# Optimization experiments

Hardware: AMD Instinct MI355X
Metric: run time of the kernel (lower is better)

The kernel has to match this reference:

```python
import jax, jax.numpy as jnp
import numpy as np

N_NODES = 50000
HIDDEN = 64
N_EDGES = 1200000


def setup_inputs() -> dict:
    key = jax.random.key(0)
    ks = jax.random.split(key, 12)
    x = jax.random.normal(ks[0], (N_NODES, HIDDEN), dtype=jnp.float32)
    edge_index = jax.random.randint(ks[1], (2, N_EDGES), 0, N_NODES, dtype=jnp.int64)
    s = 1.0 / np.sqrt(HIDDEN)
    # RGCN layer (single relation): relation weight, root weight, bias
    W_rel1 = jax.random.normal(ks[2], (HIDDEN, HIDDEN), dtype=jnp.float32) * s
    W_root1 = jax.random.normal(ks[3], (HIDDEN, HIDDEN), dtype=jnp.float32) * s
    b1 = jnp.zeros((HIDDEN,), dtype=jnp.float32)
    # Three GraphConv layers: self weight, neighbor weight, bias each
    W_self2 = jax.random.normal(ks[4], (HIDDEN, HIDDEN), dtype=jnp.float32) * s
    W_nbr2 = jax.random.normal(ks[5], (HIDDEN, HIDDEN), dtype=jnp.float32) * s
    b2 = jnp.zeros((HIDDEN,), dtype=jnp.float32)
    W_self3 = jax.random.normal(ks[6], (HIDDEN, HIDDEN), dtype=jnp.float32) * s
    W_nbr3 = jax.random.normal(ks[7], (HIDDEN, HIDDEN), dtype=jnp.float32) * s
    b3 = jnp.zeros((HIDDEN,), dtype=jnp.float32)
    W_self4 = jax.random.normal(ks[8], (HIDDEN, HIDDEN), dtype=jnp.float32) * s
    W_nbr4 = jax.random.normal(ks[9], (HIDDEN, HIDDEN), dtype=jnp.float32) * s
    b4 = jnp.zeros((HIDDEN,), dtype=jnp.float32)
    return {
        "x": x, "edge_index": edge_index,
        "W_rel1": W_rel1, "W_root1": W_root1, "b1": b1,
        "W_self2": W_self2, "W_nbr2": W_nbr2, "b2": b2,
        "W_self3": W_self3, "W_nbr3": W_nbr3, "b3": b3,
        "W_self4": W_self4, "W_nbr4": W_nbr4, "b4": b4,
    }


def _rgcn(x, W_rel, W_root, b, src, dst, n_nodes):
    # single-relation RGCN: root transform + mean-aggregated relation transform
    msg = x[src] @ W_rel                                   # [E, H]
    agg = jax.ops.segment_sum(msg, dst, num_segments=n_nodes)
    cnt = jax.ops.segment_sum(jnp.ones((src.shape[0],), x.dtype), dst, num_segments=n_nodes)
    agg = agg / jnp.maximum(cnt, 1.0)[:, None]
    return x @ W_root + agg + b


def _graphconv(x, W_self, W_nbr, b, src, dst, n_nodes):
    # GraphConv: self transform + sum-aggregated neighbor transform
    agg = jax.ops.segment_sum(x[src], dst, num_segments=n_nodes)  # [N, H]
    return x @ W_self + agg @ W_nbr + b


def reference(x, edge_index, W_rel1, W_root1, b1, W_self2, W_nbr2, b2,
              W_self3, W_nbr3, b3, W_self4, W_nbr4, b4):
    n = x.shape[0]
    src, dst = edge_index[0], edge_index[1]
    h = jax.nn.relu(_rgcn(x, W_rel1, W_root1, b1, src, dst, n))
    h = jax.nn.relu(_graphconv(h, W_self2, W_nbr2, b2, src, dst, n))
    x_1 = h
    h = jax.nn.relu(_graphconv(h, W_self3, W_nbr3, b3, src, dst, n))
    h = jax.nn.relu(_graphconv(h, W_self4, W_nbr4, b4, src, dst, n))
    x_2 = h
    return (x_1, x_2)
```

## Files before the change

### kernel.cpp

```cpp
#include <hip/hip_runtime.h>

#define N_NODES 50000
#define HIDDEN  64
#define N_EDGES 1200000

#define BSHIFT 7
#define BUKSZ  128
#define NBUK   391
#define GBIN   256
#define PAD2   4096

__device__ __forceinline__ float bcastf(float v, int k) {
    return __int_as_float(__builtin_amdgcn_readlane(__float_as_int(v), k));
}

__device__ __forceinline__ unsigned short f2bf(float x) {
    unsigned u = __float_as_uint(x);
    u += 0x7fffu + ((u >> 16) & 1u);
    return (unsigned short)(u >> 16);
}

__device__ __forceinline__ float bfl(unsigned w) { return __uint_as_float(w << 16); }
__device__ __forceinline__ float bfh(unsigned w) { return __uint_as_float(w & 0xffff0000u); }


__global__ __launch_bounds__(512) void init_kernel(int* __restrict__ cursor) {
    int tid = threadIdx.x;
    if (tid < NBUK) cursor[tid] = tid * PAD2;
}

__global__ __launch_bounds__(256) void scatter_fused_kernel(const int* __restrict__ ei,
                                                            int* __restrict__ cursor,
                                                            int* __restrict__ tmp, int E) {
    __shared__ int h[NBUK];
    __shared__ int cur[NBUK];
    int tid = threadIdx.x;
    for (int b = tid; b < NBUK; b += 256) h[b] = 0;
    __syncthreads();
    for (int e = blockIdx.x * 256 + tid; e < E; e += GBIN * 256)
        atomicAdd(&h[ei[E + e] >> BSHIFT], 1);
    __syncthreads();
    for (int b = tid; b < NBUK; b += 256) cur[b] = atomicAdd(&cursor[b], h[b]);
    __syncthreads();
    for (int e = blockIdx.x * 256 + tid; e < E; e += GBIN * 256) {
        int src = ei[e];
        int dst = ei[E + e];
        int p = atomicAdd(&cur[dst >> BSHIFT], 1);
        tmp[p] = src | ((dst & (BUKSZ - 1)) << 16);
    }
}

__global__ __launch_bounds__(512) void bucketize_kernel(const int* __restrict__ tmp,
                                                        const int* __restrict__ cursor,
                                                        int2* __restrict__ row_info,
                                                        unsigned short* __restrict__ csr,
                                                        int n) {
    __shared__ int hist[BUKSZ];
    __shared__ int cur[BUKSZ];
    __shared__ unsigned short stage[PAD2];
    int b = blockIdx.x, tid = threadIdx.x;
    int base = b * PAD2;
    int count = cursor[b] - base;
    int node_base = b << BSHIFT;

    if (tid < BUKSZ) hist[tid] = 0;
    __syncthreads();
    for (int i = tid; i < count; i += 512)
        atomicAdd(&hist[tmp[base + i] >> 16], 1);
    __syncthreads();
    int v = (tid < BUKSZ) ? hist[tid] : 0;
#pragma unroll
    for (int o = 1; o < BUKSZ; o <<= 1) {
        __syncthreads();
        int y = (tid >= o && tid < BUKSZ) ? hist[tid - o] : 0;
        __syncthreads();
        if (tid < BUKSZ) hist[tid] += y;
    }
    __syncthreads();
    if (tid < BUKSZ) {
        int excl = hist[tid] - v;
        cur[tid] = excl;
        int node = node_base + tid;
        if (node < n) row_info[node] = make_int2(base + excl, v);
    }
    __syncthreads();
    for (int i = tid; i < count; i += 512) {
        int p = tmp[base + i];
        int slot = atomicAdd(&cur[p >> 16], 1);
        stage[slot] = (unsigned short)(p & 0xFFFF);
    }
    __syncthreads();
    for (int i = tid; i < count; i += 512)
        csr[base + i] = stage[i];
}

__global__ __launch_bounds__(256) void gemm2_kernel(const float* __restrict__ h,
                                                    const float* __restrict__ Wnbr,
                                                    const float* __restrict__ Wself,
                                                    const float* __restrict__ bias,
                                                    unsigned short* __restrict__ tbf,
                                                    float* __restrict__ u, int n) {
    int lane = threadIdx.x & 63;
    float wn[64], ws[64];
#pragma unroll
    for (int k = 0; k < 64; ++k) {
        wn[k] = Wnbr[k * 64 + lane];
        ws[k] = Wself[k * 64 + lane];
    }
    float bv = bias[lane];
    int wave = (blockIdx.x * 256 + threadIdx.x) >> 6;
    int nwaves = gridDim.x * 4;
    if (wave == 0) tbf[(size_t)n * 64 + lane] = 0;
    for (int i = wave; i < n; i += nwaves) {
        float hv = h[i * 64 + lane];
        float tacc = 0.f, uacc = bv;
#pragma unroll
        for (int k = 0; k < 64; ++k) {
            float hk = bcastf(hv, k);
            tacc = fmaf(hk, wn[k], tacc);
            uacc = fmaf(hk, ws[k], uacc);
        }
        tbf[(size_t)i * 64 + lane] = f2bf(tacc);
        u[(size_t)i * 64 + lane] = uacc;
    }
}

__global__ __launch_bounds__(256) void agg_kernel(const unsigned short* __restrict__ tbf,
                                                  const float* __restrict__ u,
                                                  const int2* __restrict__ row_info,
                                                  const unsigned short* __restrict__ csr,
                                                  float* __restrict__ out, int n, int use_mean) {
    int lane = threadIdx.x & 63;
    int g = lane >> 4;
    int q = lane & 15;
    int node = (blockIdx.x * 256 + threadIdx.x) >> 6;
    if (node >= n) return;
    int2 ri = row_info[node];
    int start = ri.x, deg = ri.y;
    float4 a0 = {0,0,0,0}, a1 = {0,0,0,0}, a2 = {0,0,0,0}, a3 = {0,0,0,0};
    float4 a4 = {0,0,0,0}, a5 = {0,0,0,0}, a6 = {0,0,0,0}, a7 = {0,0,0,0};
    for (int e = 0; e < deg; e += 64) {
        int cnt = deg - e;
        if (cnt > 64) cnt = 64;
        int idx = (lane < cnt) ? (int)csr[start + e + lane] : n;
        int cnt32 = (cnt + 31) & ~31;
        for (int j = 0; j < cnt32; j += 32) {
            int s0 = __shfl(idx, j + g);
            int s1 = __shfl(idx, j + 4 + g);
            int s2 = __shfl(idx, j + 8 + g);
            int s3 = __shfl(idx, j + 12 + g);
            int s4 = __shfl(idx, j + 16 + g);
            int s5 = __shfl(idx, j + 20 + g);
            int s6 = __shfl(idx, j + 24 + g);
            int s7 = __shfl(idx, j + 28 + g);
            const uint2 w0 = *(const uint2*)(tbf + (size_t)s0 * 64 + q * 4);
            const uint2 w1 = *(const uint2*)(tbf + (size_t)s1 * 64 + q * 4);
            const uint2 w2 = *(const uint2*)(tbf + (size_t)s2 * 64 + q * 4);
            const uint2 w3 = *(const uint2*)(tbf + (size_t)s3 * 64 + q * 4);
            const uint2 w4 = *(const uint2*)(tbf + (size_t)s4 * 64 + q * 4);
            const uint2 w5 = *(const uint2*)(tbf + (size_t)s5 * 64 + q * 4);
            const uint2 w6 = *(const uint2*)(tbf + (size_t)s6 * 64 + q * 4);
            const uint2 w7 = *(const uint2*)(tbf + (size_t)s7 * 64 + q * 4);
            a0.x += bfl(w0.x); a0.y += bfh(w0.x); a0.z += bfl(w0.y); a0.w += bfh(w0.y);
            a1.x += bfl(w1.x); a1.y += bfh(w1.x); a1.z += bfl(w1.y); a1.w += bfh(w1.y);
            a2.x += bfl(w2.x); a2.y += bfh(w2.x); a2.z += bfl(w2.y); a2.w += bfh(w2.y);
            a3.x += bfl(w3.x); a3.y += bfh(w3.x); a3.z += bfl(w3.y); a3.w += bfh(w3.y);
            a4.x += bfl(w4.x); a4.y += bfh(w4.x); a4.z += bfl(w4.y); a4.w += bfh(w4.y);
            a5.x += bfl(w5.x); a5.y += bfh(w5.x); a5.z += bfl(w5.y); a5.w += bfh(w5.y);
            a6.x += bfl(w6.x); a6.y += bfh(w6.x); a6.z += bfl(w6.y); a6.w += bfh(w6.y);
            a7.x += bfl(w7.x); a7.y += bfh(w7.x); a7.z += bfl(w7.y); a7.w += bfh(w7.y);
        }
    }
    float4 acc;
    acc.x = ((a0.x + a1.x) + (a2.x + a3.x)) + ((a4.x + a5.x) + (a6.x + a7.x));
    acc.y = ((a0.y + a1.y) + (a2.y + a3.y)) + ((a4.y + a5.y) + (a6.y + a7.y));
    acc.z = ((a0.z + a1.z) + (a2.z + a3.z)) + ((a4.z + a5.z) + (a6.z + a7.z));
    acc.w = ((a0.w + a1.w) + (a2.w + a3.w)) + ((a4.w + a5.w) + (a6.w + a7.w));
    acc.x += __shfl_xor(acc.x, 16); acc.y += __shfl_xor(acc.y, 16);
    acc.z += __shfl_xor(acc.z, 16); acc.w += __shfl_xor(acc.w, 16);
    acc.x += __shfl_xor(acc.x, 32); acc.y += __shfl_xor(acc.y, 32);
    acc.z += __shfl_xor(acc.z, 32); acc.w += __shfl_xor(acc.w, 32);

    float scale = 1.f;
    if (use_mean) scale = 1.f / fmaxf((float)deg, 1.f);
    if (g == 0) {
        const float4 uv = *(const float4*)(u + (size_t)node * 64 + q * 4);
        float4 r;
        r.x = fmaxf(uv.x + acc.x * scale, 0.f);
        r.y = fmaxf(uv.y + acc.y * scale, 0.f);
        r.z = fmaxf(uv.z + acc.z * scale, 0.f);
        r.w = fmaxf(uv.w + acc.w * scale, 0.f);
        *(float4*)(out + (size_t)node * 64 + q * 4) = r;
    }
}


extern "C" void kernel_launch(void* const* d_in, const int* in_sizes, int n_in,
                              void* d_out, int out_size, void* d_ws, size_t ws_size,
                              hipStream_t stream) {
    const float* x      = (const float*)d_in[0];
    const int*   ei     = (const int*)d_in[1];
    const float* Wrel1  = (const float*)d_in[2];
    const float* Wroot1 = (const float*)d_in[3];
    const float* b1     = (const float*)d_in[4];
    const float* Wself2 = (const float*)d_in[5];
    const float* Wnbr2  = (const float*)d_in[6];
    const float* b2     = (const float*)d_in[7];
    const float* Wself3 = (const float*)d_in[8];
    const float* Wnbr3  = (const float*)d_in[9];
    const float* b3     = (const float*)d_in[10];
    const float* Wself4 = (const float*)d_in[11];
    const float* Wnbr4  = (const float*)d_in[12];
    const float* b4     = (const float*)d_in[13];

    const int N = N_NODES, E = N_EDGES;

    auto align = [](size_t o) { return (o + 255) & ~(size_t)255; };
    char* base = (char*)d_ws;
    size_t off = 0;
    int*  cursor   = (int*)(base + off);  off = align(off + (size_t)NBUK * 4);
    int2* row_info = (int2*)(base + off); off = align(off + (size_t)N_NODES * 8);
    int*  tmp      = (int*)(base + off);  off = align(off + (size_t)NBUK * PAD2 * 4);
    unsigned short* csr = (unsigned short*)(base + off); off = align(off + (size_t)NBUK * PAD2 * 2);
    unsigned short* tbf = (unsigned short*)(base + off); off = align(off + (size_t)(N + 1) * 64 * 2);
    float* u  = (float*)(base + off); off = align(off + (size_t)N * 64 * 4);
    float* h1 = (float*)(base + off); off = align(off + (size_t)N * 64 * 4);

    float* out1 = (float*)d_out;
    float* out2 = (float*)d_out + (size_t)N * 64;

    init_kernel<<<1, 512, 0, stream>>>(cursor);
    scatter_fused_kernel<<<GBIN, 256, 0, stream>>>(ei, cursor, tmp, E);
    bucketize_kernel<<<NBUK, 512, 0, stream>>>(tmp, cursor, row_info, csr, N);

    const int GB = 768;
    const int AB = (N + 3) / 4;

    gemm2_kernel<<<GB, 256, 0, stream>>>(x, Wrel1, Wroot1, b1, tbf, u, N);
    agg_kernel<<<AB, 256, 0, stream>>>(tbf, u, row_info, csr, h1, N, 1);
    gemm2_kernel<<<GB, 256, 0, stream>>>(h1, Wnbr2, Wself2, b2, tbf, u, N);
    agg_kernel<<<AB, 256, 0, stream>>>(tbf, u, row_info, csr, out1, N, 0);
    gemm2_kernel<<<GB, 256, 0, stream>>>(out1, Wnbr3, Wself3, b3, tbf, u, N);
    agg_kernel<<<AB, 256, 0, stream>>>(tbf, u, row_info, csr, h1, N, 0);
    gemm2_kernel<<<GB, 256, 0, stream>>>(h1, Wnbr4, Wself4, b4, tbf, u, N);
    agg_kernel<<<AB, 256, 0, stream>>>(tbf, u, row_info, csr, out2, N, 0);
}
```

Baseline: 336.1 us.

## Fuse aggregation with next-layer GEMM and merge CSR build with first GEMM

Replaces the separate gemm and aggregation kernels with a fused kernel that aggregates neighbours, applies relu, then immediately computes the next layer's two projections from registers using bf16 weights held in LDS. The CSR build changes from a global-atomic cursor scatter to a two-pass chunked scheme with per-chunk, per-bucket start and count matrices. It also overlaps the first GEMM and weight packing with the graph-build blocks in the same launches. This cuts the launch count and avoids writing and re-reading intermediate activations through global memory. In exchange the weights are rounded to bf16, the serial per-thread loops in build_b may be unbalanced, and the fused kernel uses a fixed grid-stride layout.

Result: slower. 616.1 us (+83.3%).

```diff
diff --git a/kernel.cpp b/kernel.cpp
--- a/kernel.cpp
+++ b/kernel.cpp
@@ -7,142 +7,184 @@
 #define BSHIFT 7
 #define BUKSZ  128
 #define NBUK   391
-#define GBIN   256
+#define ABLK   512
+#define CH     2344
 #define PAD2   4096
+#define FBLK   1024
+#define NW     (FBLK * 4)
 
 __device__ __forceinline__ float bcastf(float v, int k) {
     return __int_as_float(__builtin_amdgcn_readlane(__float_as_int(v), k));
 }
-
-__device__ __forceinline__ unsigned short f2bf(float x) {
+__device__ __forceinline__ unsigned f2bf(float x) {
     unsigned u = __float_as_uint(x);
     u += 0x7fffu + ((u >> 16) & 1u);
-    return (unsigned short)(u >> 16);
-}
-
+    return u >> 16;
+}
 __device__ __forceinline__ float bfl(unsigned w) { return __uint_as_float(w << 16); }
 __device__ __forceinline__ float bfh(unsigned w) { return __uint_as_float(w & 0xffff0000u); }
-
-
-__global__ __launch_bounds__(512) void init_kernel(int* __restrict__ cursor) {
-    int tid = threadIdx.x;
-    if (tid < NBUK) cursor[tid] = tid * PAD2;
-}
-
-__global__ __launch_bounds__(256) void scatter_fused_kernel(const int* __restrict__ ei,
-                                                            int* __restrict__ cursor,
-                                                            int* __restrict__ tmp, int E) {
-    __shared__ int h[NBUK];
+__device__ __forceinline__ void bfly(float4& a) {
+    a.x += __shfl_xor(a.x, 16); a.y += __shfl_xor(a.y, 16);
+    a.z += __shfl_xor(a.z, 16); a.w += __shfl_xor(a.w, 16);
+    a.x += __shfl_xor(a.x, 32); a.y += __shfl_xor(a.y, 32);
+    a.z += __shfl_xor(a.z, 32); a.w += __shfl_xor(a.w, 32);
+}
+
+__global__ __launch_bounds__(512) void build_a_kernel(const int* __restrict__ ei,
+                                                      int* __restrict__ tmp,
+                                                      int* __restrict__ starts_m,
+                                                      int* __restrict__ counts_m,
+                                                      const float* __restrict__ Wn2, const float* __restrict__ Ws2,
+                                                      const float* __restrict__ Wn3, const float* __restrict__ Ws3,
+                                                      const float* __restrict__ Wn4, const float* __restrict__ Ws4,
+                                                      uint4* __restrict__ pw) {
+    __shared__ int hist[NBUK];
     __shared__ int cur[NBUK];
-    int tid = threadIdx.x;
-    for (int b = tid; b < NBUK; b += 256) h[b] = 0;
-    __syncthreads();
-    for (int e = blockIdx.x * 256 + tid; e < E; e += GBIN * 256)
-        atomicAdd(&h[ei[E + e] >> BSHIFT], 1);
-    __syncthreads();
-    for (int b = tid; b < NBUK; b += 256) cur[b] = atomicAdd(&cursor[b], h[b]);
-    __syncthreads();
-    for (int e = blockIdx.x * 256 + tid; e < E; e += GBIN * 256) {
-        int src = ei[e];
-        int dst = ei[E + e];
-        int p = atomicAdd(&cur[dst >> BSHIFT], 1);
-        tmp[p] = src | ((dst & (BUKSZ - 1)) << 16);
-    }
-}
-
-__global__ __launch_bounds__(512) void bucketize_kernel(const int* __restrict__ tmp,
-                                                        const int* __restrict__ cursor,
-                                                        int2* __restrict__ row_info,
-                                                        unsigned short* __restrict__ csr,
-                                                        int n) {
+    __shared__ int stage[CH];
+    int b = blockIdx.x, tid = threadIdx.x;
+    if (b < ABLK) {
+        int base = b * CH;
+        int cnt = N_EDGES - base; if (cnt > CH) cnt = CH;
+        for (int i = tid; i < NBUK; i += 512) hist[i] = 0;
+        __syncthreads();
+        for (int i = tid; i < cnt; i += 512)
+            atomicAdd(&hist[ei[N_EDGES + base + i] >> BSHIFT], 1);
+        __syncthreads();
+        int v = (tid < NBUK) ? hist[tid] : 0;
+#pragma unroll
+        for (int o = 1; o < NBUK; o <<= 1) {
+            __syncthreads();
+            int y = (tid >= o && tid < NBUK) ? hist[tid - o] : 0;
+            __syncthreads();
+            if (tid < NBUK) hist[tid] += y;
+        }
+        __syncthreads();
+        if (tid < NBUK) {
+            int excl = hist[tid] - v;
+            cur[tid] = excl;
+            starts_m[tid * ABLK + b] = base + excl;
+            counts_m[tid * ABLK + b] = v;
+        }
+        __syncthreads();
+        for (int i = tid; i < cnt; i += 512) {
+            int src = ei[base + i];
+            int dst = ei[N_EDGES + base + i];
+            int p = atomicAdd(&cur[dst >> BSHIFT], 1);
+            stage[p] = src | ((dst & (BUKSZ - 1)) << 16);
+        }
+        __syncthreads();
+        for (int i = tid; i < cnt; i += 512) tmp[base + i] = stage[i];
+    } else {
+        int layer = b - ABLK;
+        const float* Wn = (layer == 0) ? Wn2 : (layer == 1) ? Wn3 : Wn4;
+        const float* Ws = (layer == 0) ? Ws2 : (layer == 1) ? Ws3 : Ws4;
+        for (int e = tid; e < 1024; e += 512) {
+            const float4 a = *(const float4*)(Wn + e * 4);
+            const float4 c = *(const float4*)(Ws + e * 4);
+            uint4 o;
+            o.x = f2bf(a.x) | (f2bf(a.y) << 16);
+            o.y = f2bf(a.z) | (f2bf(a.w) << 16);
+            o.z = f2bf(c.x) | (f2bf(c.y) << 16);
+            o.w = f2bf(c.z) | (f2bf(c.w) << 16);
+            pw[layer * 1024 + e] = o;
+        }
+    }
+}
+
+__global__ __launch_bounds__(512) void build_b_kernel(const int* __restrict__ tmp,
+                                                      const int* __restrict__ starts_m,
+                                                      const int* __restrict__ counts_m,
+                                                      int2* __restrict__ row_info,
+                                                      unsigned short* __restrict__ csr,
+                                                      const float* __restrict__ x,
+                                                      const float* __restrict__ Wrel,
+                                                      const float* __restrict__ Wroot,
+                                                      const float* __restrict__ bias,
+                                                      unsigned short* __restrict__ tbf,
+                                                      float* __restrict__ u) {
+    __shared__ int sl[ABLK];
+    __shared__ int cl[ABLK];
     __shared__ int hist[BUKSZ];
     __shared__ int cur[BUKSZ];
     __shared__ unsigned short stage[PAD2];
     int b = blockIdx.x, tid = threadIdx.x;
-    int base = b * PAD2;
-    int count = cursor[b] - base;
-    int node_base = b << BSHIFT;
-
-    if (tid < BUKSZ) hist[tid] = 0;
-    __syncthreads();
-    for (int i = tid; i < count; i += 512)
-        atomicAdd(&hist[tmp[base + i] >> 16], 1);
-    __syncthreads();
-    int v = (tid < BUKSZ) ? hist[tid] : 0;
-#pragma unroll
-    for (int o = 1; o < BUKSZ; o <<= 1) {
-        __syncthreads();
-        int y = (tid >= o && tid < BUKSZ) ? hist[tid - o] : 0;
-        __syncthreads();
-        if (tid < BUKSZ) hist[tid] += y;
-    }
-    __syncthreads();
-    if (tid < BUKSZ) {
-        int excl = hist[tid] - v;
-        cur[tid] = excl;
-        int node = node_base + tid;
-        if (node < n) row_info[node] = make_int2(base + excl, v);
-    }
-    __syncthreads();
-    for (int i = tid; i < count; i += 512) {
-        int p = tmp[base + i];
-        int slot = atomicAdd(&cur[p >> 16], 1);
-        stage[slot] = (unsigned short)(p & 0xFFFF);
-    }
-    __syncthreads();
-    for (int i = tid; i < count; i += 512)
-        csr[base + i] = stage[i];
-}
-
-__global__ __launch_bounds__(256) void gemm2_kernel(const float* __restrict__ h,
-                                                    const float* __restrict__ Wnbr,
-                                                    const float* __restrict__ Wself,
-                                                    const float* __restrict__ bias,
-                                                    unsigned short* __restrict__ tbf,
-                                                    float* __restrict__ u, int n) {
-    int lane = threadIdx.x & 63;
-    float wn[64], ws[64];
-#pragma unroll
-    for (int k = 0; k < 64; ++k) {
-        wn[k] = Wnbr[k * 64 + lane];
-        ws[k] = Wself[k * 64 + lane];
-    }
-    float bv = bias[lane];
-    int wave = (blockIdx.x * 256 + threadIdx.x) >> 6;
-    int nwaves = gridDim.x * 4;
-    if (wave == 0) tbf[(size_t)n * 64 + lane] = 0;
-    for (int i = wave; i < n; i += nwaves) {
-        float hv = h[i * 64 + lane];
-        float tacc = 0.f, uacc = bv;
+    if (b < NBUK) {
+        sl[tid] = starts_m[b * ABLK + tid];
+        cl[tid] = counts_m[b * ABLK + tid];
+        if (tid < BUKSZ) hist[tid] = 0;
+        __syncthreads();
+        {
+            int s = sl[tid], c = cl[tid];
+            for (int i = 0; i < c; ++i) atomicAdd(&hist[tmp[s + i] >> 16], 1);
+        }
+        __syncthreads();
+        int v = (tid < BUKSZ) ? hist[tid] : 0;
+#pragma unroll
+        for (int o = 1; o < BUKSZ; o <<= 1) {
+            __syncthreads();
+            int y = (tid >= o && tid < BUKSZ) ? hist[tid - o] : 0;
+            __syncthreads();
+            if (tid < BUKSZ) hist[tid] += y;
+        }
+        __syncthreads();
+        if (tid < BUKSZ) {
+            int excl = hist[tid] - v;
+            cur[tid] = excl;
+            int node = (b << BSHIFT) + tid;
+            if (node < N_NODES) row_info[node] = make_int2(b * PAD2 + excl, v);
+        }
+        __syncthreads();
+        {
+            int s = sl[tid], c = cl[tid];
+            for (int i = 0; i < c; ++i) {
+                int p = tmp[s + i];
+                int slot = atomicAdd(&cur[p >> 16], 1);
+                stage[slot] = (unsigned short)(p & 0xFFFF);
+            }
+        }
+        __syncthreads();
+        int total = hist[BUKSZ - 1];
+        for (int i = tid; i < total; i += 512) csr[b * PAD2 + i] = stage[i];
+    } else {
+        int lane = tid & 63;
+        float wn[64], ws[64];
 #pragma unroll
         for (int k = 0; k < 64; ++k) {
-            float hk = bcastf(hv, k);
-            tacc = fmaf(hk, wn[k], tacc);
-            uacc = fmaf(hk, ws[k], uacc);
-        }
-        tbf[(size_t)i * 64 + lane] = f2bf(tacc);
-        u[(size_t)i * 64 + lane] = uacc;
-    }
-}
-
-__global__ __launch_bounds__(256) void agg_kernel(const unsigned short* __restrict__ tbf,
-                                                  const float* __restrict__ u,
-                                                  const int2* __restrict__ row_info,
-                                                  const unsigned short* __restrict__ csr,
-                                                  float* __restrict__ out, int n, int use_mean) {
-    int lane = threadIdx.x & 63;
-    int g = lane >> 4;
-    int q = lane & 15;
-    int node = (blockIdx.x * 256 + threadIdx.x) >> 6;
-    if (node >= n) return;
+            wn[k] = Wrel[k * 64 + lane];
+            ws[k] = Wroot[k * 64 + lane];
+        }
+        float bv = bias[lane];
+        int wave = (b - NBUK) * 8 + (tid >> 6);
+        int nwaves = (gridDim.x - NBUK) * 8;
+        if (wave == 0) tbf[(size_t)N_NODES * 64 + lane] = 0;
+        for (int i = wave; i < N_NODES; i += nwaves) {
+            float hv = x[i * 64 + lane];
+            float tacc = 0.f, uacc = bv;
+#pragma unroll
+            for (int k = 0; k < 64; ++k) {
+                float hk = bcastf(hv, k);
+                tacc = fmaf(hk, wn[k], tacc);
+                uacc = fmaf(hk, ws[k], uacc);
+            }
+            tbf[(size_t)i * 64 + lane] = (unsigned short)f2bf(tacc);
+            u[(size_t)i * 64 + lane] = uacc;
+        }
+    }
+}
+
+__device__ __forceinline__ float4 agg_node(const unsigned short* __restrict__ tin,
+                                           const float* __restrict__ uin,
+                                           const int2* __restrict__ row_info,
+                                           const unsigned short* __restrict__ csr,
+                                           int node, int lane, int g, int q, int use_mean) {
+    if (node >= N_NODES) return make_float4(0.f, 0.f, 0.f, 0.f);
     int2 ri = row_info[node];
     int start = ri.x, deg = ri.y;
-    float4 a0 = {0,0,0,0}, a1 = {0,0,0,0}, a2 = {0,0,0,0}, a3 = {0,0,0,0};
-    float4 a4 = {0,0,0,0}, a5 = {0,0,0,0}, a6 = {0,0,0,0}, a7 = {0,0,0,0};
+    float4 a0{0,0,0,0}, a1{0,0,0,0}, a2{0,0,0,0}, a3{0,0,0,0};
+    float4 a4{0,0,0,0}, a5{0,0,0,0}, a6{0,0,0,0}, a7{0,0,0,0};
     for (int e = 0; e < deg; e += 64) {
-        int cnt = deg - e;
-        if (cnt > 64) cnt = 64;
-        int idx = (lane < cnt) ? (int)csr[start + e + lane] : n;
+        int cnt = deg - e; if (cnt > 64) cnt = 64;
+        int idx = (lane < cnt) ? (int)csr[start + e + lane] : N_NODES;
         int cnt32 = (cnt + 31) & ~31;
         for (int j = 0; j < cnt32; j += 32) {
             int s0 = __shfl(idx, j + g);
@@ -153,14 +195,14 @@
             int s5 = __shfl(idx, j + 20 + g);
             int s6 = __shfl(idx, j + 24 + g);
             int s7 = __shfl(idx, j + 28 + g);
-            const uint2 w0 = *(const uint2*)(tbf + (size_t)s0 * 64 + q * 4);
-            const uint2 w1 = *(const uint2*)(tbf + (size_t)s1 * 64 + q * 4);
-            const uint2 w2 = *(const uint2*)(tbf + (size_t)s2 * 64 + q * 4);
-            const uint2 w3 = *(const uint2*)(tbf + (size_t)s3 * 64 + q * 4);
-            const uint2 w4 = *(const uint2*)(tbf + (size_t)s4 * 64 + q * 4);
-            const uint2 w5 = *(const uint2*)(tbf + (size_t)s5 * 64 + q * 4);
-            const uint2 w6 = *(const uint2*)(tbf + (size_t)s6 * 64 + q * 4);
-            const uint2 w7 = *(const uint2*)(tbf + (size_t)s7 * 64 + q * 4);
+            const uint2 w0 = *(const uint2*)(tin + (size_t)s0 * 64 + q * 4);
+            const uint2 w1 = *(const uint2*)(tin + (size_t)s1 * 64 + q * 4);
+            const uint2 w2 = *(const uint2*)(tin + (size_t)s2 * 64 + q * 4);
+            const uint2 w3 = *(const uint2*)(tin + (size_t)s3 * 64 + q * 4);
+            const uint2 w4 = *(const uint2*)(tin + (size_t)s4 * 64 + q * 4);
+            const uint2 w5 = *(const uint2*)(tin + (size_t)s5 * 64 + q * 4);
+            const uint2 w6 = *(const uint2*)(tin + (size_t)s6 * 64 + q * 4);
+            const uint2 w7 = *(const uint2*)(tin + (size_t)s7 * 64 + q * 4);
             a0.x += bfl(w0.x); a0.y += bfh(w0.x); a0.z += bfl(w0.y); a0.w += bfh(w0.y);
             a1.x += bfl(w1.x); a1.y += bfh(w1.x); a1.z += bfl(w1.y); a1.w += bfh(w1.y);
             a2.x += bfl(w2.x); a2.y += bfh(w2.x); a2.z += bfl(w2.y); a2.w += bfh(w2.y);
@@ -176,24 +218,93 @@
     acc.y = ((a0.y + a1.y) + (a2.y + a3.y)) + ((a4.y + a5.y) + (a6.y + a7.y));
     acc.z = ((a0.z + a1.z) + (a2.z + a3.z)) + ((a4.z + a5.z) + (a6.z + a7.z));
     acc.w = ((a0.w + a1.w) + (a2.w + a3.w)) + ((a4.w + a5.w) + (a6.w + a7.w));
-    acc.x += __shfl_xor(acc.x, 16); acc.y += __shfl_xor(acc.y, 16);
-    acc.z += __shfl_xor(acc.z, 16); acc.w += __shfl_xor(acc.w, 16);
-    acc.x += __shfl_xor(acc.x, 32); acc.y += __shfl_xor(acc.y, 32);
-    acc.z += __shfl_xor(acc.z, 32); acc.w += __shfl_xor(acc.w, 32);
-
-    float scale = 1.f;
-    if (use_mean) scale = 1.f / fmaxf((float)deg, 1.f);
-    if (g == 0) {
-        const float4 uv = *(const float4*)(u + (size_t)node * 64 + q * 4);
-        float4 r;
-        r.x = fmaxf(uv.x + acc.x * scale, 0.f);
-        r.y = fmaxf(uv.y + acc.y * scale, 0.f);
-        r.z = fmaxf(uv.z + acc.z * scale, 0.f);
-        r.w = fmaxf(uv.w + acc.w * scale, 0.f);
-        *(float4*)(out + (size_t)node * 64 + q * 4) = r;
-    }
-}
-
+    bfly(acc);
+    float sc = use_mean ? 1.f / fmaxf((float)deg, 1.f) : 1.f;
+    const float4 uv = *(const float4*)(uin + (size_t)node * 64 + q * 4);
+    float4 h;
+    h.x = fmaxf(uv.x + acc.x * sc, 0.f);
+    h.y = fmaxf(uv.y + acc.y * sc, 0.f);
+    h.z = fmaxf(uv.z + acc.z * sc, 0.f);
+    h.w = fmaxf(uv.w + acc.w * sc, 0.f);
+    return h;
+}
+
+__global__ __launch_bounds__(256) void fused_kernel(const unsigned short* __restrict__ tin,
+                                                    const float* __restrict__ uin,
+                                                    const int2* __restrict__ row_info,
+                                                    const unsigned short* __restrict__ csr,
+                                                    const uint4* __restrict__ pwL,
+                                                    const float* __restrict__ bias_next,
+                                                    unsigned short* __restrict__ tout,
+                                                    float* __restrict__ uout,
+                                                    float* __restrict__ dout,
+                                                    int use_mean, int do_gemm) {
+    __shared__ uint4 wlds[1024];
+    __shared__ float blds[64];
+    int tid = threadIdx.x;
+    if (do_gemm) {
+        for (int i = tid; i < 1024; i += 256) wlds[i] = pwL[i];
+        if (tid < 64) blds[tid] = bias_next[tid];
+        if (blockIdx.x == 0 && tid < 32)
+            ((uint4*)(tout + (size_t)N_NODES * 64))[tid % 8 + (tid / 8) * 0] = make_uint4(0,0,0,0);
+        if (blockIdx.x == 0 && tid < 64)
+            ((unsigned int*)(tout + (size_t)N_NODES * 64))[tid] = 0;
+    }
+    __syncthreads();
+    int lane = tid & 63, g = lane >> 4, q = lane & 15;
+    int w = blockIdx.x * 4 + (tid >> 6);
+
+#pragma unroll
+    for (int bi = 0; bi < 4; ++bi) {
+        int nodes[4];
+        float4 h4[4];
+#pragma unroll
+        for (int i = 0; i < 4; ++i) {
+            int node = w + NW * (bi * 4 + i);
+            nodes[i] = node;
+            h4[i] = agg_node(tin, uin, row_info, csr, node, lane, g, q, use_mean);
+            if (dout && node < N_NODES && g == 0)
+                *(float4*)(dout + (size_t)node * 64 + q * 4) = h4[i];
+        }
+        if (!do_gemm) continue;
+        float4 tp[4] = {{0,0,0,0},{0,0,0,0},{0,0,0,0},{0,0,0,0}};
+        float4 up[4] = {{0,0,0,0},{0,0,0,0},{0,0,0,0},{0,0,0,0}};
+#pragma unroll
+        for (int j = 0; j < 16; ++j) {
+            uint4 wv = wlds[(16 * g + j) * 16 + q];
+            float wn0 = bfl(wv.x), wn1 = bfh(wv.x), wn2 = bfl(wv.y), wn3 = bfh(wv.y);
+            float ws0 = bfl(wv.z), ws1 = bfh(wv.z), ws2 = bfl(wv.w), ws3 = bfh(wv.w);
+            int src = g * 4 + (j >> 2);
+#pragma unroll
+            for (int i = 0; i < 4; ++i) {
+                float hk;
+                if ((j & 3) == 0)      hk = __shfl(h4[i].x, src);
+                else if ((j & 3) == 1) hk = __shfl(h4[i].y, src);
+                else if ((j & 3) == 2) hk = __shfl(h4[i].z, src);
+                else                   hk = __shfl(h4[i].w, src);
+                tp[i].x = fmaf(hk, wn0, tp[i].x); tp[i].y = fmaf(hk, wn1, tp[i].y);
+                tp[i].z = fmaf(hk, wn2, tp[i].z); tp[i].w = fmaf(hk, wn3, tp[i].w);
+                up[i].x = fmaf(hk, ws0, up[i].x); up[i].y = fmaf(hk, ws1, up[i].y);
+                up[i].z = fmaf(hk, ws2, up[i].z); up[i].w = fmaf(hk, ws3, up[i].w);
+            }
+        }
+#pragma unroll
+        for (int i = 0; i < 4; ++i) {
+            bfly(tp[i]); bfly(up[i]);
+            if (nodes[i] < N_NODES && g == 0) {
+                const float4 bv = *(const float4*)&blds[q * 4];
+                float4 uo;
+                uo.x = up[i].x + bv.x; uo.y = up[i].y + bv.y;
+                uo.z = up[i].z + bv.z; uo.w = up[i].w + bv.w;
+                *(float4*)(uout + (size_t)nodes[i] * 64 + q * 4) = uo;
+                uint2 tpk;
+                tpk.x = f2bf(tp[i].x) | (f2bf(tp[i].y) << 16);
+                tpk.y = f2bf(tp[i].z) | (f2bf(tp[i].w) << 16);
+                *(uint2*)(tout + (size_t)nodes[i] * 64 + q * 4) = tpk;
+            }
+        }
+    }
+}
 
 extern "C" void kernel_launch(void* const* d_in, const int* in_sizes, int n_in,
                               void* d_out, int out_size, void* d_ws, size_t ws_size,
@@ -213,35 +324,31 @@
     const float* Wnbr4  = (const float*)d_in[12];
     const float* b4     = (const float*)d_in[13];
 
-    const int N = N_NODES, E = N_EDGES;
+    const int N = N_NODES;
 
     auto align = [](size_t o) { return (o + 255) & ~(size_t)255; };
     char* base = (char*)d_ws;
     size_t off = 0;
-    int*  cursor   = (int*)(base + off);  off = align(off + (size_t)NBUK * 4);
-    int2* row_info = (int2*)(base + off); off = align(off + (size_t)N_NODES * 8);
-    int*  tmp      = (int*)(base + off);  off = align(off + (size_t)NBUK * PAD2 * 4);
+    int*  tmp      = (int*)(base + off);  off = align(off + (size_t)ABLK * CH * 4);
+    int*  starts_m = (int*)(base + off);  off = align(off + (size_t)NBUK * ABLK * 4);
+    int*  counts_m = (int*)(base + off);  off = align(off + (size_t)NBUK * ABLK * 4);
+    int2* row_info = (int2*)(base + off); off = align(off + (size_t)N * 8);
     unsigned short* csr = (unsigned short*)(base + off); off = align(off + (size_t)NBUK * PAD2 * 2);
-    unsigned short* tbf = (unsigned short*)(base + off); off = align(off + (size_t)(N + 1) * 64 * 2);
-    float* u  = (float*)(base + off); off = align(off + (size_t)N * 64 * 4);
-    float* h1 = (float*)(base + off); off = align(off + (size_t)N * 64 * 4);
+    uint4* pw = (uint4*)(base + off);     off = align(off + (size_t)3 * 1024 * 16);
+    unsigned short* tbA = (unsigned short*)(base + off); off = align(off + (size_t)(N + 1) * 64 * 2);
+    unsigned short* tbB = (unsigned short*)(base + off); off = align(off + (size_t)(N + 1) * 64 * 2);
+    float* uA = (float*)(base + off); off = align(off + (size_t)N * 64 * 4);
+    float* uB = (float*)(base + off); off = align(off + (size_t)N * 64 * 4);
 
     float* out1 = (float*)d_out;
     float* out2 = (float*)d_out + (size_t)N * 64;
 
-    init_kernel<<<1, 512, 0, stream>>>(cursor);
-    scatter_fused_kernel<<<GBIN, 256, 0, stream>>>(ei, cursor, tmp, E);
-    bucketize_kernel<<<NBUK, 512, 0, stream>>>(tmp, cursor, row_info, csr, N);
-
-    const int GB = 768;
-    const int AB = (N + 3) / 4;
-
-    gemm2_kernel<<<GB, 256, 0, stream>>>(x, Wrel1, Wroot1, b1, tbf, u, N);
-    agg_kernel<<<AB, 256, 0, stream>>>(tbf, u, row_info, csr, h1, N, 1);
-    gemm2_kernel<<<GB, 256, 0, stream>>>(h1, Wnbr2, Wself2, b2, tbf, u, N);
-    agg_kernel<<<AB, 256, 0, stream>>>(tbf, u, row_info, csr, out1, N, 0);
-    gemm2_kernel<<<GB, 256, 0, stream>>>(out1, Wnbr3, Wself3, b3, tbf, u, N);
-    agg_kernel<<<AB, 256, 0, stream>>>(tbf, u, row_info, csr, h1, N, 0);
-    gemm2_kernel<<<GB, 256, 0, stream>>>(h1, Wnbr4, Wself4, b4, tbf, u, N);
-    agg_kernel<<<AB, 256, 0, stream>>>(tbf, u, row_info, csr, out2, N, 0);
-}
+    build_a_kernel<<<ABLK + 3, 512, 0, stream>>>(ei, tmp, starts_m, counts_m,
+                                                 Wnbr2, Wself2, Wnbr3, Wself3, Wnbr4, Wself4, pw);
+    build_b_kernel<<<NBUK + 1024, 512, 0, stream>>>(tmp, starts_m, counts_m, row_info, csr,
+                                                    x, Wrel1, Wroot1, b1, tbA, uA);
+    fused_kernel<<<FBLK, 256, 0, stream>>>(tbA, uA, row_info, csr, pw,        b2, tbB, uB, nullptr, 1, 1);
+    fused_kernel<<<FBLK, 256, 0, stream>>>(tbB, uB, row_info, csr, pw + 1024, b3, tbA, uA, out1, 0, 1);
+    fused_kernel<<<FBLK, 256, 0, stream>>>(tbA, uA, row_info, csr, pw + 2048, b4, tbB, uB, nullptr, 0, 1);
+    fused_kernel<<<FBLK, 256, 0, stream>>>(tbB, uB, row_info, csr, nullptr, nullptr, nullptr, nullptr, out2, 0, 0);
+}
```
